# Kernel tuning notes

Hardware: AMD Instinct MI355X
Metric: run time of the kernel (lower is better)

Reference implementation:

```python
import jax, jax.numpy as jnp
import numpy as np

N = 100000
E = 1600000
H = 8
D_IN = 128
D_HEAD = 16  # output_dim // n_heads


def setup_inputs() -> dict:
    key = jax.random.key(0)
    ks = jax.random.split(key, 8)
    x = jax.random.normal(ks[0], (N, D_IN), dtype=jnp.float32)
    W = jax.random.normal(ks[1], (H, D_IN, D_HEAD), dtype=jnp.float32) * 0.05
    a1 = jax.random.normal(ks[2], (H, D_HEAD), dtype=jnp.float32) * 0.1
    b1 = jnp.zeros((H,), dtype=jnp.float32)
    a2 = jax.random.normal(ks[3], (H, D_HEAD), dtype=jnp.float32) * 0.1
    b2 = jnp.zeros((H,), dtype=jnp.float32)
    src = jnp.sort(jax.random.randint(ks[4], (E,), 0, N)).astype(jnp.int32)
    dst = jax.random.randint(ks[5], (E,), 0, N).astype(jnp.int32)
    return {"x": x, "W": W, "a1": a1, "b1": b1, "a2": a2, "b2": b2,
            "src": src, "dst": dst}


def _gat_forward(x, W, a1, b1, a2, b2, src, dst):
    n = x.shape[0]
    # per-head linear transform: [H, N, D_HEAD]
    feats = jnp.einsum('nd,hdo->hno', x, W)
    # per-node attention scalars (1x1 conv with bias): [H, N]
    f1 = jnp.einsum('hno,ho->hn', feats, a1) + b1[:, None]
    f2 = jnp.einsum('hno,ho->hn', feats, a2) + b2[:, None]
    # edge logits: logit[e] = f1[src[e]] + f2[dst[e]]  -> [E, H]
    e = f1[:, src].T + f2[:, dst].T
    e = jnp.maximum(0.2 * e, e)  # leaky_relu
    # sparse row-softmax over each source node's neighbors (segment softmax)
    m = jax.ops.segment_max(e, src, num_segments=n)           # [N, H]
    ex = jnp.exp(e - m[src])                                   # [E, H]
    denom = jax.ops.segment_sum(ex, src, num_segments=n)      # [N, H]
    coef = ex / denom[src]                                     # [E, H]
    # spmm: out[i] = sum_{j in N(i)} coef[ij] * feats[j]
    feats_nhd = jnp.transpose(feats, (1, 0, 2))                # [N, H, D_HEAD]
    msg = coef[:, :, None] * feats_nhd[dst]                    # [E, H, D_HEAD]
    out = jax.ops.segment_sum(msg, src, num_segments=n)       # [N, H, D_HEAD]
    out = out.reshape(n, H * D_HEAD)
    return jax.nn.elu(out)


def reference(x, W, a1, b1, a2, b2, src, dst):
    return _gat_forward(x, W, a1, b1, a2, b2, src, dst)
```

## Files before the change

### kernel.cpp

```cpp
#include <hip/hip_runtime.h>
#include <hip/hip_bf16.h>
#include <math.h>

#define HEADS 8
#define D_IN 128
#define D_HEAD 16
#define D_OUT 128

typedef unsigned short ushort_t;
typedef unsigned int uint_t;
typedef __attribute__((ext_vector_type(8))) short short8;
typedef __attribute__((ext_vector_type(4))) float floatx4;

static __device__ inline uint_t f32_to_bf16(float f) {
    uint_t u = __float_as_uint(f);
    return (u + 0x7fffu + ((u >> 16) & 1u)) >> 16;
}
static __device__ inline uint_t pack_bf16(float lo, float hi) {
    return (f32_to_bf16(hi) << 16) | f32_to_bf16(lo);
}
static __device__ inline float bf_lo(uint_t p) { return __uint_as_float(p << 16); }
static __device__ inline float bf_hi(uint_t p) { return __uint_as_float(p & 0xffff0000u); }

#define PREP_WBLOCKS 64
__global__ __launch_bounds__(256) void prep_kernel(
    const float* __restrict__ Wg, ushort_t* __restrict__ Wfrag,
    const int* __restrict__ src, int* __restrict__ row_ptr, int n, int e)
{
    if (blockIdx.x < PREP_WBLOCKS) {
        int t = blockIdx.x * 256 + threadIdx.x;
        int j    = t & 7;
        int lane = (t >> 3) & 63;
        int ks   = (t >> 9) & 3;
        int ct   = t >> 11;
        int k = ks * 32 + (lane >> 4) * 8 + j;
        int m = lane & 15;
        float v = Wg[(size_t)ct * (D_IN * D_HEAD) + k * D_HEAD + m];
        Wfrag[t] = (ushort_t)f32_to_bf16(v);
    } else {
        int i = (blockIdx.x - PREP_WBLOCKS) * 256 + threadIdx.x;
        if (i > n) return;
        int lo = 0, hi = e;
        while (lo < hi) {
            int mid = (lo + hi) >> 1;
            if (src[mid] < i) lo = mid + 1; else hi = mid;
        }
        row_ptr[i] = lo;
    }
}

__global__ __launch_bounds__(256) void gemm_feats_mfma(
    const float* __restrict__ x, const ushort_t* __restrict__ Wfrag,
    const float* __restrict__ a1, const float* __restrict__ b1,
    const float* __restrict__ a2, const float* __restrict__ b2,
    ushort_t* __restrict__ feats, float* __restrict__ f1,
    float* __restrict__ f2, int n)
{
    __shared__ ushort_t Xs[128][136];

    const int tid  = threadIdx.x;
    const int wave = tid >> 6;
    const int lane = tid & 63;
    const int row0 = blockIdx.x * 128;

#pragma unroll
    for (int it = 0; it < 16; ++it) {
        int idx = it * 256 + tid;
        int r   = idx >> 5;
        int c4  = (idx & 31) * 4;
        float4 v = make_float4(0.f, 0.f, 0.f, 0.f);
        if (row0 + r < n) v = *(const float4*)(x + (size_t)(row0 + r) * D_IN + c4);
        *(uint2*)&Xs[r][c4] = make_uint2(pack_bf16(v.x, v.y), pack_bf16(v.z, v.w));
    }
    __syncthreads();

    const int m  = lane & 15;
    const int kg = lane >> 4;

    floatx4 acc[2][8];
#pragma unroll
    for (int nt = 0; nt < 2; ++nt)
#pragma unroll
        for (int ct = 0; ct < 8; ++ct) acc[nt][ct] = (floatx4){0.f, 0.f, 0.f, 0.f};

#pragma unroll
    for (int ks = 0; ks < 4; ++ks) {
        short8 xb0 = *(const short8*)&Xs[wave * 32 + m][ks * 32 + kg * 8];
        short8 xb1 = *(const short8*)&Xs[wave * 32 + 16 + m][ks * 32 + kg * 8];
#pragma unroll
        for (int ct = 0; ct < 8; ++ct) {
            short8 wa = *(const short8*)(Wfrag + ((size_t)(ct * 4 + ks) * 64 + lane) * 8);
            acc[0][ct] = __builtin_amdgcn_mfma_f32_16x16x32_bf16(wa, xb0, acc[0][ct], 0, 0, 0);
            acc[1][ct] = __builtin_amdgcn_mfma_f32_16x16x32_bf16(wa, xb1, acc[1][ct], 0, 0, 0);
        }
    }

#pragma unroll
    for (int nt = 0; nt < 2; ++nt) {
        const int node = row0 + wave * 32 + nt * 16 + m;
        const bool valid = node < n;
        if (valid) {
#pragma unroll
            for (int ct = 0; ct < 8; ++ct) {
                uint_t lo = pack_bf16(acc[nt][ct][0], acc[nt][ct][1]);
                uint_t hi = pack_bf16(acc[nt][ct][2], acc[nt][ct][3]);
                *(uint2*)(feats + (size_t)node * D_OUT + ct * 16 + kg * 4) = make_uint2(lo, hi);
            }
        }
#pragma unroll
        for (int ct = 0; ct < 8; ++ct) {
            float4 A1 = *(const float4*)(a1 + ct * D_HEAD + kg * 4);
            float4 A2 = *(const float4*)(a2 + ct * D_HEAD + kg * 4);
            float p1 = acc[nt][ct][0] * A1.x + acc[nt][ct][1] * A1.y +
                       acc[nt][ct][2] * A1.z + acc[nt][ct][3] * A1.w;
            float p2 = acc[nt][ct][0] * A2.x + acc[nt][ct][1] * A2.y +
                       acc[nt][ct][2] * A2.z + acc[nt][ct][3] * A2.w;
            p1 += __shfl_xor(p1, 16); p1 += __shfl_xor(p1, 32);
            p2 += __shfl_xor(p2, 16); p2 += __shfl_xor(p2, 32);
            if (kg == 0 && valid) {
                f1[(size_t)node * HEADS + ct] = p1 + b1[ct];
                f2[(size_t)node * HEADS + ct] = p2 + b2[ct];
            }
        }
    }
}

__global__ __launch_bounds__(256) void aggregate_kernel(
    const int* __restrict__ row_ptr, const int* __restrict__ dst,
    const ushort_t* __restrict__ feats,
    const float* __restrict__ f1, const float* __restrict__ f2,
    float* __restrict__ out, int n)
{
    int node = blockIdx.x * 4 + (threadIdx.x >> 6);
    node = __builtin_amdgcn_readfirstlane(node);
    if (node >= n) return;
    const int lane = threadIdx.x & 63;
    const int h = lane >> 3;

    const float f1v   = f1[(size_t)node * HEADS + h];
    const int   start = row_ptr[node];
    const int   end   = row_ptr[node + 1];

    const float*    f2h = f2 + h;
    const ushort_t* fl  = feats + 2 * lane;

    float s = 0.f, ax = 0.f, ay = 0.f;
    int e = start;
    for (; e + 8 <= end; e += 8) {
        int d[8]; float g[8]; uint_t p[8];
#pragma unroll
        for (int q = 0; q < 8; ++q) d[q] = dst[e + q];
#pragma unroll
        for (int q = 0; q < 8; ++q) {
            g[q] = f2h[d[q] * HEADS];
            p[q] = *(const uint_t*)(fl + d[q] * D_OUT);
        }
#pragma unroll
        for (int q = 0; q < 8; ++q) {
            float z = f1v + g[q];
            z = fmaxf(z, 0.2f * z);
            float w = __expf(z);
            s += w;
            ax = fmaf(w, bf_lo(p[q]), ax);
            ay = fmaf(w, bf_hi(p[q]), ay);
        }
    }
    for (; e < end; ++e) {
        const int d = dst[e];
        const float g = f2h[d * HEADS];
        const uint_t p = *(const uint_t*)(fl + d * D_OUT);
        float z = f1v + g;
        z = fmaxf(z, 0.2f * z);
        const float w = __expf(z);
        s += w;
        ax = fmaf(w, bf_lo(p), ax);
        ay = fmaf(w, bf_hi(p), ay);
    }

    float rx = 0.f, ry = 0.f;
    if (end > start) {
        rx = ax / s;
        ry = ay / s;
        rx = rx > 0.f ? rx : expm1f(rx);
        ry = ry > 0.f ? ry : expm1f(ry);
    }
    *(float2*)(out + (size_t)node * D_OUT + 2 * lane) = make_float2(rx, ry);
}

extern "C" void kernel_launch(void* const* d_in, const int* in_sizes, int n_in,
                              void* d_out, int out_size, void* d_ws, size_t ws_size,
                              hipStream_t stream)
{
    const float* x  = (const float*)d_in[0];
    const float* W  = (const float*)d_in[1];
    const float* a1 = (const float*)d_in[2];
    const float* b1 = (const float*)d_in[3];
    const float* a2 = (const float*)d_in[4];
    const float* b2 = (const float*)d_in[5];
    const int* src  = (const int*)d_in[6];
    const int* dst  = (const int*)d_in[7];
    float* out = (float*)d_out;

    const int n = in_sizes[0] / D_IN;
    const int e = in_sizes[6];

    char* ws = (char*)d_ws;
    size_t off = 0;
    ushort_t* feats = (ushort_t*)(ws + off);
    off += (size_t)n * D_OUT * sizeof(ushort_t); off = (off + 255) & ~(size_t)255;
    float* f1 = (float*)(ws + off);
    off += (size_t)n * HEADS * sizeof(float);    off = (off + 255) & ~(size_t)255;
    float* f2 = (float*)(ws + off);
    off += (size_t)n * HEADS * sizeof(float);    off = (off + 255) & ~(size_t)255;
    int* row_ptr = (int*)(ws + off);
    off += (size_t)(n + 1) * sizeof(int);        off = (off + 255) & ~(size_t)255;
    ushort_t* Wfrag = (ushort_t*)(ws + off);

    dim3 blk(256);
    const int rp_blocks = (n + 1 + 255) / 256;
    prep_kernel<<<dim3(PREP_WBLOCKS + rp_blocks), blk, 0, stream>>>(
        W, Wfrag, src, row_ptr, n, e);
    gemm_feats_mfma<<<dim3((n + 127) / 128), blk, 0, stream>>>(
        x, Wfrag, a1, b1, a2, b2, feats, f1, f2, n);
    aggregate_kernel<<<dim3((n + 3) / 4), blk, 0, stream>>>(
        row_ptr, dst, feats, f1, f2, out, n);
}
```

Before: 220.9 us.

## Build row_ptr by edge-boundary scatter and share edge weights across lanes via shuffle

The row_ptr construction changes from a per-node binary search over src to a per-edge scatter, where each edge writes row_ptr for every node between its predecessor's source and its own. In the aggregation loop, each lane now computes the attention weight for one of 8 edges per head (8 gathers and exps per lane instead of 64 lanes each doing 8). The weights are then broadcast with __shfl. This cuts redundant f2 gathers and exp work but adds shuffles, and the prep kernel now launches more blocks (over edges rather than nodes).

```diff
diff --git a/kernel.cpp b/kernel.cpp
--- a/kernel.cpp
+++ b/kernel.cpp
@@ -39,13 +39,10 @@
         Wfrag[t] = (ushort_t)f32_to_bf16(v);
     } else {
         int i = (blockIdx.x - PREP_WBLOCKS) * 256 + threadIdx.x;
-        if (i > n) return;
-        int lo = 0, hi = e;
-        while (lo < hi) {
-            int mid = (lo + hi) >> 1;
-            if (src[mid] < i) lo = mid + 1; else hi = mid;
-        }
-        row_ptr[i] = lo;
+        if (i > e) return;
+        int sp = (i == 0) ? -1 : src[i - 1];
+        int sc = (i == e) ? n  : src[i];
+        for (int node = sp + 1; node <= sc; ++node) row_ptr[node] = i;
     }
 }
 
@@ -141,34 +138,35 @@
     const int   start = row_ptr[node];
     const int   end   = row_ptr[node + 1];
 
-    const float*    f2h = f2 + h;
-    const ushort_t* fl  = feats + 2 * lane;
+    const ushort_t* fl = feats + 2 * lane;
 
     float s = 0.f, ax = 0.f, ay = 0.f;
     int e = start;
     for (; e + 8 <= end; e += 8) {
-        int d[8]; float g[8]; uint_t p[8];
+        int d[8];
 #pragma unroll
         for (int q = 0; q < 8; ++q) d[q] = dst[e + q];
+        const int   dq = dst[e + (lane & 7)];
+        const float g  = f2[(size_t)dq * HEADS + h];
+        float z = f1v + g;
+        z = fmaxf(z, 0.2f * z);
+        const float w = __expf(z);
+        uint_t p[8];
+#pragma unroll
+        for (int q = 0; q < 8; ++q)
+            p[q] = *(const uint_t*)(fl + (size_t)d[q] * D_OUT);
 #pragma unroll
         for (int q = 0; q < 8; ++q) {
-            g[q] = f2h[d[q] * HEADS];
-            p[q] = *(const uint_t*)(fl + d[q] * D_OUT);
-        }
-#pragma unroll
-        for (int q = 0; q < 8; ++q) {
-            float z = f1v + g[q];
-            z = fmaxf(z, 0.2f * z);
-            float w = __expf(z);
-            s += w;
-            ax = fmaf(w, bf_lo(p[q]), ax);
-            ay = fmaf(w, bf_hi(p[q]), ay);
+            const float wq = __shfl(w, (lane & 56) | q);
+            s += wq;
+            ax = fmaf(wq, bf_lo(p[q]), ax);
+            ay = fmaf(wq, bf_hi(p[q]), ay);
         }
     }
     for (; e < end; ++e) {
         const int d = dst[e];
-        const float g = f2h[d * HEADS];
-        const uint_t p = *(const uint_t*)(fl + d * D_OUT);
+        const float g = f2[(size_t)d * HEADS + h];
+        const uint_t p = *(const uint_t*)(fl + (size_t)d * D_OUT);
         float z = f1v + g;
         z = fmaxf(z, 0.2f * z);
         const float w = __expf(z);
@@ -217,7 +215,7 @@
     ushort_t* Wfrag = (ushort_t*)(ws + off);
 
     dim3 blk(256);
-    const int rp_blocks = (n + 1 + 255) / 256;
+    const int rp_blocks = (e + 1 + 255) / 256;
     prep_kernel<<<dim3(PREP_WBLOCKS + rp_blocks), blk, 0, stream>>>(
         W, Wfrag, src, row_ptr, n, e);
     gemm_feats_mfma<<<dim3((n + 127) / 128), blk, 0, stream>>>(
```

Result: no change. 217.6 us (-1.5%).
